# Optimization experiments

Measured on AMD Instinct MI355X. Metric: run time of the kernel, lower is better.

## Reference

```python
import jax, jax.numpy as jnp
import numpy as np

N, E, F, H, C, G = 50000, 800000, 128, 1, 64, 256
NEG_SLOPE = 0.2


def _seg_softmax(e, seg, n):
    # numerically-stable softmax over edges grouped by target node
    m = jax.ops.segment_max(e, seg, num_segments=n)
    ex = jnp.exp(e - m[seg])
    s = jax.ops.segment_sum(ex, seg, num_segments=n)
    return ex / (s[seg] + 1e-16)


def _gatv2(x, src, dst, wl, bl, wr, br, att, bo, n):
    # GATv2Conv (PyG semantics): lin_l on source x_j, lin_r on target x_i
    xl = (x @ wl.T + bl).reshape(n, H, C)
    xr = (x @ wr.T + br).reshape(n, H, C)
    s = xl[src] + xr[dst]                      # [E, H, C]
    e = jnp.sum(jax.nn.leaky_relu(s, NEG_SLOPE) * att, axis=-1)  # [E, H]
    alpha = _seg_softmax(e, dst, n)
    out = jax.ops.segment_sum(alpha[..., None] * xl[src], dst, num_segments=n)
    return out.reshape(n, H * C) + bo


def setup_inputs() -> dict:
    key = jax.random.key(0)
    ks = jax.random.split(key, 24)
    d = {}
    d['x'] = jax.random.normal(ks[0], (N, F), dtype=jnp.float32)
    d['edge_index'] = jax.random.randint(ks[1], (2, E), 0, N)
    d['batch_idx'] = jnp.sort(jax.random.randint(ks[2], (N,), 0, G))
    sc = 0.1
    # conv1: in=F, out=C
    d['wl1'] = jax.random.normal(ks[3], (H * C, F)) * sc
    d['bl1'] = jnp.zeros((H * C,), jnp.float32)
    d['wr1'] = jax.random.normal(ks[4], (H * C, F)) * sc
    d['br1'] = jnp.zeros((H * C,), jnp.float32)
    d['att1'] = jax.random.normal(ks[5], (H, C)) * sc
    d['bo1'] = jnp.zeros((H * C,), jnp.float32)
    # conv2, conv3: in=H*C, out=C
    d['wl2'] = jax.random.normal(ks[6], (H * C, H * C)) * sc
    d['bl2'] = jnp.zeros((H * C,), jnp.float32)
    d['wr2'] = jax.random.normal(ks[7], (H * C, H * C)) * sc
    d['br2'] = jnp.zeros((H * C,), jnp.float32)
    d['att2'] = jax.random.normal(ks[8], (H, C)) * sc
    d['bo2'] = jnp.zeros((H * C,), jnp.float32)
    d['wl3'] = jax.random.normal(ks[9], (H * C, H * C)) * sc
    d['bl3'] = jnp.zeros((H * C,), jnp.float32)
    d['wr3'] = jax.random.normal(ks[10], (H * C, H * C)) * sc
    d['br3'] = jnp.zeros((H * C,), jnp.float32)
    d['att3'] = jax.random.normal(ks[11], (H, C)) * sc
    d['bo3'] = jnp.zeros((H * C,), jnp.float32)
    # heads
    d['lin1_w'] = jax.random.normal(ks[12], (C, 3 * H * C)) * sc
    d['lin1_b'] = jnp.zeros((C,), jnp.float32)
    d['pred_w'] = jax.random.normal(ks[13], (C, C)) * sc
    d['pred_b'] = jnp.zeros((C,), jnp.float32)
    d['cls_w'] = jax.random.normal(ks[14], (2, C)) * sc
    d['cls_b'] = jnp.zeros((2,), jnp.float32)
    return d


def reference(x, edge_index, batch_idx, wl1, bl1, wr1, br1, att1, bo1,
              wl2, bl2, wr2, br2, att2, bo2, wl3, bl3, wr3, br3, att3, bo3,
              lin1_w, lin1_b, pred_w, pred_b, cls_w, cls_b):
    # add self-loops (GATv2Conv default add_self_loops=True)
    loop = jnp.arange(N, dtype=edge_index.dtype)
    src = jnp.concatenate([edge_index[0], loop])
    dst = jnp.concatenate([edge_index[1], loop])
    x1 = jax.nn.relu(_gatv2(x, src, dst, wl1, bl1, wr1, br1, att1, bo1, N))
    x2 = jax.nn.relu(_gatv2(x1, src, dst, wl2, bl2, wr2, br2, att2, bo2, N))
    x3 = jax.nn.relu(_gatv2(x2, src, dst, wl3, bl3, wr3, br3, att3, bo3, N))
    h = jax.nn.relu(jnp.concatenate([x1, x2, x3], axis=1) @ lin1_w.T + lin1_b)
    g = jax.ops.segment_sum(h, batch_idx, num_segments=G)  # global_add_pool
    emb = jax.nn.relu(g @ pred_w.T + pred_b)                # pred_layer
    out = emb @ cls_w.T + cls_b                             # cls_layer
    return out
```

## Files before the change

### kernel.cpp

```cpp
#include <hip/hip_runtime.h>
#include <hip/hip_bf16.h>

#define N_NODES 50000
#define N_EDGES 800000
#define FDIM 128
#define CDIM 64
#define NGRAPH 256
#define LRELU_SLOPE 0.2f
#define NBUCK ((N_NODES + 255) / 256)
#define BCAP 5120
#define ABLK 400
#define EPB ((N_EDGES + ABLK - 1) / ABLK)
#define NDBIN 64

typedef unsigned short ushort_t;
typedef unsigned int uint_t;
typedef __attribute__((ext_vector_type(8))) short short8v;
typedef __attribute__((ext_vector_type(4))) float float4v;

__device__ __forceinline__ ushort_t f2bf(float f) {
    uint_t u = __float_as_uint(f);
    u += 0x7FFFu + ((u >> 16) & 1u);
    return (ushort_t)(u >> 16);
}
__device__ __forceinline__ float bf2f(ushort_t u) {
    return __uint_as_float(((uint_t)u) << 16);
}

__device__ __forceinline__ float fast_exp2(float x) {
    return __builtin_amdgcn_exp2f(x);
}

__device__ __forceinline__ int wave_incl_scan(int v, int lane) {
#pragma unroll
    for (int off = 1; off < 64; off <<= 1) {
        int t = __shfl_up(v, off);
        if (lane >= off) v += t;
    }
    return v;
}

__device__ __forceinline__ float wave_sum(float v) {
#pragma unroll
    for (int off = 32; off >= 1; off >>= 1) v += __shfl_xor(v, off);
    return v;
}

__global__ void k_bucket(const int* __restrict__ src, const int* __restrict__ dst,
                         int* __restrict__ bcnt, int2* __restrict__ stage) {
    __shared__ int lhist[NBUCK];
    __shared__ int lbase[NBUCK];
    __shared__ int lcur[NBUCK];
    int tid = threadIdx.x;
    int e0 = blockIdx.x * EPB;
    int e1 = min(e0 + EPB, N_EDGES);
    for (int t = tid; t < NBUCK; t += 256) { lhist[t] = 0; lcur[t] = 0; }
    __syncthreads();
    for (int e = e0 + tid; e < e1; e += 256)
        atomicAdd(&lhist[dst[e] >> 8], 1);
    __syncthreads();
    for (int t = tid; t < NBUCK; t += 256)
        lbase[t] = atomicAdd(&bcnt[t], lhist[t]);
    __syncthreads();
    for (int e = e0 + tid; e < e1; e += 256) {
        int s = src[e], d = dst[e];
        int b = d >> 8;
        int loff = atomicAdd(&lcur[b], 1);
        int pos = lbase[b] + loff;
        if (pos < BCAP) stage[(size_t)b * BCAP + pos] = make_int2(s, d);
    }
}

__global__ void k_bscan(const int* __restrict__ bcnt, int* __restrict__ bbase) {
    __shared__ int wsum[4];
    int tid = threadIdx.x;
    int lane = tid & 63, w = tid >> 6;
    int v = (tid < NBUCK) ? bcnt[tid] : 0;
    int incl = wave_incl_scan(v, lane);
    if (lane == 63) wsum[w] = incl;
    __syncthreads();
    if (tid == 0) {
        int s = 0;
#pragma unroll
        for (int k = 0; k < 4; k++) { int t = wsum[k]; wsum[k] = s; s += t; }
    }
    __syncthreads();
    if (tid < NBUCK) bbase[tid] = incl - v + wsum[w];
}

__global__ void k_csr(const int* __restrict__ bcnt, const int* __restrict__ bbase,
                      const int2* __restrict__ stage, int* __restrict__ rowptr,
                      int* __restrict__ cnt, int* __restrict__ dhist,
                      int* __restrict__ csr_src) {
    __shared__ int lcnt[256];
    __shared__ int lcur[256];
    __shared__ int ldh[NDBIN];
    __shared__ int wsum[4];
    int b = blockIdx.x;
    int tid = threadIdx.x;
    int lane = tid & 63, w = tid >> 6;
    lcnt[tid] = 0;
    if (tid < NDBIN) ldh[tid] = 0;
    __syncthreads();
    int n = min(bcnt[b], BCAP);
    const int2* sp = stage + (size_t)b * BCAP;
    for (int i = tid; i < n; i += 256)
        atomicAdd(&lcnt[sp[i].y & 255], 1);
    __syncthreads();
    int v = lcnt[tid];
    int incl = wave_incl_scan(v, lane);
    if (lane == 63) wsum[w] = incl;
    __syncthreads();
    if (tid == 0) {
        int s = 0;
#pragma unroll
        for (int k = 0; k < 4; k++) { int t = wsum[k]; wsum[k] = s; s += t; }
    }
    __syncthreads();
    int excl = incl - v + wsum[w];
    int bb = bbase[b];
    int node = (b << 8) + tid;
    if (node < N_NODES) {
        rowptr[node] = bb + excl;
        cnt[node] = v;
        atomicAdd(&ldh[min(v, NDBIN - 1)], 1);
    }
    lcur[tid] = excl;
    __syncthreads();
    if (tid < NDBIN && ldh[tid]) atomicAdd(&dhist[tid], ldh[tid]);
    if (b == 0 && tid == 0) rowptr[N_NODES] = N_EDGES;
    for (int i = tid; i < n; i += 256) {
        int2 sd = sp[i];
        int pos = atomicAdd(&lcur[sd.y & 255], 1);
        csr_src[bb + pos] = sd.x;
    }
}

__global__ void k_scan2d(const int* __restrict__ dhist, int* __restrict__ dcur) {
    int lane = threadIdx.x;
    int v = dhist[lane];
    int incl = wave_incl_scan(v, lane);
    dcur[lane] = incl - v;
}

__global__ void k_dscatter(const int* __restrict__ cnt, int* __restrict__ dcur,
                           int* __restrict__ order) {
    __shared__ int lh[NDBIN], lb[NDBIN], lc[NDBIN];
    int b = blockIdx.x, tid = threadIdx.x;
    if (tid < NDBIN) { lh[tid] = 0; lc[tid] = 0; }
    __syncthreads();
    int node = b * 256 + tid;
    bool ok = node < N_NODES;
    int dg = ok ? min(cnt[node], NDBIN - 1) : 0;
    if (ok) atomicAdd(&lh[dg], 1);
    __syncthreads();
    if (tid < NDBIN) lb[tid] = lh[tid] ? atomicAdd(&dcur[tid], lh[tid]) : 0;
    __syncthreads();
    if (ok) {
        int off2 = atomicAdd(&lc[dg], 1);
        order[lb[dg] + off2] = node;
    }
}

struct WSrc {
    const float* s[7];
    int off[8];
};
__global__ void k_cvt_w(WSrc ws, ushort_t* __restrict__ hi, ushort_t* __restrict__ lo) {
    int gid = blockIdx.x * 256 + threadIdx.x;
    int stride = gridDim.x * 256;
#pragma unroll
    for (int mi = 0; mi < 7; mi++) {
        int n = ws.off[mi + 1] - ws.off[mi];
        const float* s = ws.s[mi];
        ushort_t* h = hi + ws.off[mi];
        ushort_t* l = lo + ws.off[mi];
        for (int i = gid; i < n; i += stride) {
            float f = s[i];
            ushort_t hb = f2bf(f);
            h[i] = hb;
            l[i] = f2bf(f - bf2f(hb));
        }
    }
}

template <int K, bool A_FP32>
__global__ void k_gemm_dual_mfma(const void* __restrict__ xa,
                                 const ushort_t* __restrict__ wlh, const ushort_t* __restrict__ wll,
                                 const ushort_t* __restrict__ wrh, const ushort_t* __restrict__ wrl,
                                 const float* __restrict__ bl, const float* __restrict__ br,
                                 ushort_t* __restrict__ xl, ushort_t* __restrict__ xr) {
    int tid = threadIdx.x;
    int wv = tid >> 6, lane = tid & 63;
    int m0 = blockIdx.x * 64 + wv * 16;
    if (m0 >= N_NODES) return;
    int arow = min(m0 + (lane & 15), N_NODES - 1);
    int koff = (lane >> 4) * 8;
    int wrow = lane & 15;

    float4v acc[8];
#pragma unroll
    for (int f = 0; f < 8; f++) acc[f] = (float4v)(0.f);

#pragma unroll
    for (int k0 = 0; k0 < K; k0 += 32) {
        short8v afrag;
        if (A_FP32) {
            const float* ap = (const float*)xa + (size_t)arow * K + k0 + koff;
            float4 a0 = *reinterpret_cast<const float4*>(ap);
            float4 a1 = *reinterpret_cast<const float4*>(ap + 4);
            afrag[0] = (short)f2bf(a0.x); afrag[1] = (short)f2bf(a0.y);
            afrag[2] = (short)f2bf(a0.z); afrag[3] = (short)f2bf(a0.w);
            afrag[4] = (short)f2bf(a1.x); afrag[5] = (short)f2bf(a1.y);
            afrag[6] = (short)f2bf(a1.z); afrag[7] = (short)f2bf(a1.w);
        } else {
            afrag = *reinterpret_cast<const short8v*>((const ushort_t*)xa + (size_t)arow * K + k0 + koff);
        }
#pragma unroll
        for (int f = 0; f < 8; f++) {
            const ushort_t* bh = (f < 4) ? wlh : wrh;
            const ushort_t* blo = (f < 4) ? wll : wrl;
            int row = ((f * 16 + wrow) & 63);
            size_t boff = (size_t)row * K + k0 + koff;
            short8v bfh = *reinterpret_cast<const short8v*>(bh + boff);
            short8v bfl = *reinterpret_cast<const short8v*>(blo + boff);
            acc[f] = __builtin_amdgcn_mfma_f32_16x16x32_bf16(afrag, bfh, acc[f], 0, 0, 0);
            acc[f] = __builtin_amdgcn_mfma_f32_16x16x32_bf16(afrag, bfl, acc[f], 0, 0, 0);
        }
    }

    int r0 = m0 + (lane >> 4) * 4;
#pragma unroll
    for (int f = 0; f < 8; f++) {
        int col = f * 16 + (lane & 15);
        float bias = (col < 64) ? bl[col] : br[col - 64];
        ushort_t* dstp = (col < 64) ? xl : xr;
        int c = col & 63;
#pragma unroll
        for (int j = 0; j < 4; j++) {
            int row = r0 + j;
            if (row < N_NODES) dstp[(size_t)row * 64 + c] = f2bf(acc[f][j] + bias);
        }
    }
}

__global__ void k_gemm_h_pool(const ushort_t* __restrict__ x1, const ushort_t* __restrict__ x2,
                              const ushort_t* __restrict__ x3,
                              const ushort_t* __restrict__ whi, const ushort_t* __restrict__ wlo,
                              const float* __restrict__ b, const int* __restrict__ batch,
                              float* __restrict__ g) {
    __shared__ float ht[64][65];
    int tid = threadIdx.x;
    int wv = tid >> 6, lane = tid & 63;
    int m0 = blockIdx.x * 64 + wv * 16;
    bool wactive = m0 < N_NODES;

    if (wactive) {
        int arow = min(m0 + (lane & 15), N_NODES - 1);
        int koff = (lane >> 4) * 8;
        int wrow = lane & 15;
        float4v acc[4];
#pragma unroll
        for (int f = 0; f < 4; f++) acc[f] = (float4v)(0.f);
#pragma unroll
        for (int ks = 0; ks < 6; ks++) {
            int k0 = ks * 32;
            const ushort_t* srcp = (ks < 2) ? x1 : (ks < 4 ? x2 : x3);
            int kc = k0 & 63;
            short8v afrag = *reinterpret_cast<const short8v*>(srcp + (size_t)arow * 64 + kc + koff);
#pragma unroll
            for (int f = 0; f < 4; f++) {
                size_t boff = (size_t)(f * 16 + wrow) * 192 + k0 + koff;
                short8v bfh = *reinterpret_cast<const short8v*>(whi + boff);
                short8v bfl = *reinterpret_cast<const short8v*>(wlo + boff);
                acc[f] = __builtin_amdgcn_mfma_f32_16x16x32_bf16(afrag, bfh, acc[f], 0, 0, 0);
                acc[f] = __builtin_amdgcn_mfma_f32_16x16x32_bf16(afrag, bfl, acc[f], 0, 0, 0);
            }
        }
        int r0 = wv * 16 + (lane >> 4) * 4;
#pragma unroll
        for (int f = 0; f < 4; f++) {
            int col = f * 16 + (lane & 15);
            float bias = b[col];
#pragma unroll
            for (int j = 0; j < 4; j++) {
                float o = acc[f][j] + bias;
                ht[r0 + j][col] = o > 0.f ? o : 0.f;
            }
        }
    }
    __syncthreads();

    int c = tid & 63, rr = tid >> 6;
    int blkbase = blockIdx.x * 64;
    float acc = 0.f;
    int cur = -1;
    for (int r = rr; r < 64; r += 4) {
        int node = blkbase + r;
        if (node >= N_NODES) break;
        int bb = batch[node];
        if (bb != cur) {
            if (cur >= 0) atomicAdd(&g[cur * 64 + c], acc);
            cur = bb;
            acc = 0.f;
        }
        acc += ht[r][c];
    }
    if (cur >= 0) atomicAdd(&g[cur * 64 + c], acc);
}

__global__ void k_gat(const ushort_t* __restrict__ xl, const ushort_t* __restrict__ xr,
                      const int* __restrict__ rowptr, const int* __restrict__ csr_src,
                      const int* __restrict__ order,
                      const float* __restrict__ att, const float* __restrict__ bo,
                      ushort_t* __restrict__ xout) {
    int tid = threadIdx.x;
    int wv = tid >> 6, lane = tid & 63;
    int gl = lane & 15;
    int slot = blockIdx.x * 16 + wv * 4 + (lane >> 4);
    if (slot >= N_NODES) return;
    int node = order[slot];
    const float LOG2E = 1.44269504f;
    int c0 = gl * 4;
    float4 a4 = *reinterpret_cast<const float4*>(att + c0);
    float at0 = a4.x * LOG2E, at1 = a4.y * LOG2E, at2 = a4.z * LOG2E, at3 = a4.w * LOG2E;
    size_t nb = (size_t)node * 64 + c0;
    ushort4 qr = *reinterpret_cast<const ushort4*>(xr + nb);
    ushort4 ql = *reinterpret_cast<const ushort4*>(xl + nb);
    float xr0 = bf2f(qr.x), xr1 = bf2f(qr.y), xr2 = bf2f(qr.z), xr3 = bf2f(qr.w);
    float l0 = bf2f(ql.x), l1 = bf2f(ql.y), l2 = bf2f(ql.z), l3 = bf2f(ql.w);

    auto grd = [](float p) {
        p += __shfl_xor(p, 1);
        p += __shfl_xor(p, 2);
        p += __shfl_xor(p, 4);
        p += __shfl_xor(p, 8);
        return p;
    };
    auto score4 = [&](float v0, float v1, float v2, float v3) {
        float s0 = v0 + xr0, s1 = v1 + xr1, s2 = v2 + xr2, s3 = v3 + xr3;
        float t0 = fmaxf(s0, LRELU_SLOPE * s0);
        float t1 = fmaxf(s1, LRELU_SLOPE * s1);
        float t2 = fmaxf(s2, LRELU_SLOPE * s2);
        float t3 = fmaxf(s3, LRELU_SLOPE * s3);
        return ((t0 * at0 + t1 * at1) + (t2 * at2 + t3 * at3));
    };

    int beg = rowptr[node], end = rowptr[node + 1];
    int deg = end - beg;
    int lim = end - 1;

    float m = grd(score4(l0, l1, l2, l3));
    float ssum = 1.f;
    float a0 = l0, a1 = l1, a2 = l2, a3 = l3;

    for (int j = 0; j < deg; j += 8) {
        int base = beg + j;
        int i0 = base;
        int i1 = min(base + 1, lim), i2 = min(base + 2, lim), i3 = min(base + 3, lim);
        int i4 = min(base + 4, lim), i5 = min(base + 5, lim);
        int i6 = min(base + 6, lim), i7 = min(base + 7, lim);
        int s0 = csr_src[i0], s1 = csr_src[i1], s2 = csr_src[i2], s3 = csr_src[i3];
        int s4 = csr_src[i4], s5 = csr_src[i5], s6 = csr_src[i6], s7 = csr_src[i7];
        ushort4 q0 = *reinterpret_cast<const ushort4*>(xl + (size_t)s0 * 64 + c0);
        ushort4 q1 = *reinterpret_cast<const ushort4*>(xl + (size_t)s1 * 64 + c0);
        ushort4 q2 = *reinterpret_cast<const ushort4*>(xl + (size_t)s2 * 64 + c0);
        ushort4 q3 = *reinterpret_cast<const ushort4*>(xl + (size_t)s3 * 64 + c0);
        ushort4 q4 = *reinterpret_cast<const ushort4*>(xl + (size_t)s4 * 64 + c0);
        ushort4 q5 = *reinterpret_cast<const ushort4*>(xl + (size_t)s5 * 64 + c0);
        ushort4 q6 = *reinterpret_cast<const ushort4*>(xl + (size_t)s6 * 64 + c0);
        ushort4 q7 = *reinterpret_cast<const ushort4*>(xl + (size_t)s7 * 64 + c0);
        float v00 = bf2f(q0.x), v01 = bf2f(q0.y), v02 = bf2f(q0.z), v03 = bf2f(q0.w);
        float v10 = bf2f(q1.x), v11 = bf2f(q1.y), v12 = bf2f(q1.z), v13 = bf2f(q1.w);
        float v20 = bf2f(q2.x), v21 = bf2f(q2.y), v22 = bf2f(q2.z), v23 = bf2f(q2.w);
        float v30 = bf2f(q3.x), v31 = bf2f(q3.y), v32 = bf2f(q3.z), v33 = bf2f(q3.w);
        float v40 = bf2f(q4.x), v41 = bf2f(q4.y), v42 = bf2f(q4.z), v43 = bf2f(q4.w);
        float v50 = bf2f(q5.x), v51 = bf2f(q5.y), v52 = bf2f(q5.z), v53 = bf2f(q5.w);
        float v60 = bf2f(q6.x), v61 = bf2f(q6.y), v62 = bf2f(q6.z), v63 = bf2f(q6.w);
        float v70 = bf2f(q7.x), v71 = bf2f(q7.y), v72 = bf2f(q7.z), v73 = bf2f(q7.w);
        float e0 = grd(score4(v00, v01, v02, v03));
        float e1 = grd(score4(v10, v11, v12, v13));
        float e2 = grd(score4(v20, v21, v22, v23));
        float e3 = grd(score4(v30, v31, v32, v33));
        float e4 = grd(score4(v40, v41, v42, v43));
        float e5 = grd(score4(v50, v51, v52, v53));
        float e6 = grd(score4(v60, v61, v62, v63));
        float e7 = grd(score4(v70, v71, v72, v73));
        int rem = deg - j;
        if (rem < 8) {
            e1 = (rem > 1) ? e1 : -1e30f;
            e2 = (rem > 2) ? e2 : -1e30f;
            e3 = (rem > 3) ? e3 : -1e30f;
            e4 = (rem > 4) ? e4 : -1e30f;
            e5 = (rem > 5) ? e5 : -1e30f;
            e6 = (rem > 6) ? e6 : -1e30f;
            e7 = (rem > 7) ? e7 : -1e30f;
        }
        float mx = fmaxf(fmaxf(fmaxf(e0, e1), fmaxf(e2, e3)),
                         fmaxf(fmaxf(e4, e5), fmaxf(e6, e7)));
        float mn = fmaxf(m, mx);
        float sc = fast_exp2(m - mn);
        float w0 = fast_exp2(e0 - mn), w1 = fast_exp2(e1 - mn);
        float w2 = fast_exp2(e2 - mn), w3 = fast_exp2(e3 - mn);
        float w4 = fast_exp2(e4 - mn), w5 = fast_exp2(e5 - mn);
        float w6 = fast_exp2(e6 - mn), w7 = fast_exp2(e7 - mn);
        ssum = ssum * sc + (((w0 + w1) + (w2 + w3)) + ((w4 + w5) + (w6 + w7)));
        a0 = a0 * sc + (((w0 * v00 + w1 * v10) + (w2 * v20 + w3 * v30)) +
                        ((w4 * v40 + w5 * v50) + (w6 * v60 + w7 * v70)));
        a1 = a1 * sc + (((w0 * v01 + w1 * v11) + (w2 * v21 + w3 * v31)) +
                        ((w4 * v41 + w5 * v51) + (w6 * v61 + w7 * v71)));
        a2 = a2 * sc + (((w0 * v02 + w1 * v12) + (w2 * v22 + w3 * v32)) +
                        ((w4 * v42 + w5 * v52) + (w6 * v62 + w7 * v72)));
        a3 = a3 * sc + (((w0 * v03 + w1 * v13) + (w2 * v23 + w3 * v33)) +
                        ((w4 * v43 + w5 * v53) + (w6 * v63 + w7 * v73)));
        m = mn;
    }

    float rs = 1.f / (ssum + 1e-16f);
    float4 b4 = *reinterpret_cast<const float4*>(bo + c0);
    float o0 = fmaxf(a0 * rs + b4.x, 0.f);
    float o1 = fmaxf(a1 * rs + b4.y, 0.f);
    float o2 = fmaxf(a2 * rs + b4.z, 0.f);
    float o3 = fmaxf(a3 * rs + b4.w, 0.f);
    ushort4 oq;
    oq.x = f2bf(o0); oq.y = f2bf(o1); oq.z = f2bf(o2); oq.w = f2bf(o3);
    *reinterpret_cast<ushort4*>(xout + nb) = oq;
}

__global__ void k_head(const float* __restrict__ g, const float* __restrict__ pw,
                       const float* __restrict__ pb, const float* __restrict__ cw,
                       const float* __restrict__ cb, float* __restrict__ out) {
    int gb = blockIdx.x;
    int c = threadIdx.x;
    const float* gr = g + gb * 64;
    float a = pb[c];
    const float* pwr = pw + c * 64;
#pragma unroll
    for (int k = 0; k < 64; k++) a += gr[k] * pwr[k];
    a = a > 0.f ? a : 0.f;
    float o0 = wave_sum(a * cw[c]);
    float o1 = wave_sum(a * cw[64 + c]);
    if (c == 0) {
        out[gb * 2 + 0] = o0 + cb[0];
        out[gb * 2 + 1] = o1 + cb[1];
    }
}

extern "C" void kernel_launch(void* const* d_in, const int* in_sizes, int n_in,
                              void* d_out, int out_size, void* d_ws, size_t ws_size,
                              hipStream_t stream) {
    const float* x    = (const float*)d_in[0];
    const int*   ei   = (const int*)d_in[1];
    const int*   bidx = (const int*)d_in[2];
    const float* wl1 = (const float*)d_in[3],  *bl1 = (const float*)d_in[4];
    const float* wr1 = (const float*)d_in[5],  *br1 = (const float*)d_in[6];
    const float* att1 = (const float*)d_in[7], *bo1 = (const float*)d_in[8];
    const float* wl2 = (const float*)d_in[9],  *bl2 = (const float*)d_in[10];
    const float* wr2 = (const float*)d_in[11], *br2 = (const float*)d_in[12];
    const float* att2 = (const float*)d_in[13], *bo2 = (const float*)d_in[14];
    const float* wl3 = (const float*)d_in[15], *bl3 = (const float*)d_in[16];
    const float* wr3 = (const float*)d_in[17], *br3 = (const float*)d_in[18];
    const float* att3 = (const float*)d_in[19], *bo3 = (const float*)d_in[20];
    const float* lw = (const float*)d_in[21], *lb = (const float*)d_in[22];
    const float* pw = (const float*)d_in[23], *pb = (const float*)d_in[24];
    const float* cw = (const float*)d_in[25], *cb = (const float*)d_in[26];
    float* out = (float*)d_out;

    char* wsb = (char*)d_ws;
    size_t off = 0;
    auto alloc = [&](size_t bytes) {
        void* p = wsb + off;
        off = (off + bytes + 255) & ~(size_t)255;
        return p;
    };
    int* cnt      = (int*)alloc((size_t)N_NODES * 4);
    int* rowptr   = (int*)alloc((size_t)(N_NODES + 1) * 4);
    int* bcnt     = (int*)alloc((size_t)(NBUCK + NDBIN) * 4);
    int* dhist    = bcnt + NBUCK;
    int* bbase    = (int*)alloc((size_t)NBUCK * 4);
    int* dcur     = (int*)alloc((size_t)NDBIN * 4);
    int* order    = (int*)alloc((size_t)N_NODES * 4);
    int2* stage   = (int2*)alloc((size_t)NBUCK * BCAP * 8);
    int* csr_src  = (int*)alloc((size_t)N_EDGES * 4);
    const int woff[8] = {0, 8192, 16384, 20480, 24576, 28672, 32768, 45056};
    ushort_t* whi = (ushort_t*)alloc((size_t)45056 * 2);
    ushort_t* wlo = (ushort_t*)alloc((size_t)45056 * 2);
    ushort_t* xl   = (ushort_t*)alloc((size_t)N_NODES * 64 * 2);
    ushort_t* xrr  = (ushort_t*)alloc((size_t)N_NODES * 64 * 2);
    ushort_t* x1b  = (ushort_t*)alloc((size_t)N_NODES * 64 * 2);
    ushort_t* x2b  = (ushort_t*)alloc((size_t)N_NODES * 64 * 2);
    ushort_t* x3b  = (ushort_t*)alloc((size_t)N_NODES * 64 * 2);
    float* g      = (float*)alloc((size_t)NGRAPH * 64 * 4);
    (void)ws_size; (void)in_sizes; (void)n_in; (void)out_size;

    const int* srcp = ei;
    const int* dstp = ei + N_EDGES;

    hipMemsetAsync(bcnt, 0, (size_t)(NBUCK + NDBIN) * 4, stream);
    hipMemsetAsync(g, 0, (size_t)NGRAPH * 64 * 4, stream);

    k_bucket<<<ABLK, 256, 0, stream>>>(srcp, dstp, bcnt, stage);
    k_bscan<<<1, 256, 0, stream>>>(bcnt, bbase);
    k_csr<<<NBUCK, 256, 0, stream>>>(bcnt, bbase, stage, rowptr, cnt, dhist, csr_src);
    k_scan2d<<<1, 64, 0, stream>>>(dhist, dcur);
    k_dscatter<<<NBUCK, 256, 0, stream>>>(cnt, dcur, order);

    WSrc ws;
    ws.s[0] = wl1; ws.s[1] = wr1; ws.s[2] = wl2; ws.s[3] = wr2;
    ws.s[4] = wl3; ws.s[5] = wr3; ws.s[6] = lw;
    for (int i = 0; i < 8; i++) ws.off[i] = woff[i];
    k_cvt_w<<<64, 256, 0, stream>>>(ws, whi, wlo);

    int gemmBlocks = (N_NODES + 63) / 64;
    int gatBlocks = (N_NODES + 15) / 16;

    k_gemm_dual_mfma<128, true><<<gemmBlocks, 256, 0, stream>>>(
        x, whi + woff[0], wlo + woff[0], whi + woff[1], wlo + woff[1], bl1, br1, xl, xrr);
    k_gat<<<gatBlocks, 256, 0, stream>>>(xl, xrr, rowptr, csr_src, order, att1, bo1, x1b);
    k_gemm_dual_mfma<64, false><<<gemmBlocks, 256, 0, stream>>>(
        x1b, whi + woff[2], wlo + woff[2], whi + woff[3], wlo + woff[3], bl2, br2, xl, xrr);
    k_gat<<<gatBlocks, 256, 0, stream>>>(xl, xrr, rowptr, csr_src, order, att2, bo2, x2b);
    k_gemm_dual_mfma<64, false><<<gemmBlocks, 256, 0, stream>>>(
        x2b, whi + woff[4], wlo + woff[4], whi + woff[5], wlo + woff[5], bl3, br3, xl, xrr);
    k_gat<<<gatBlocks, 256, 0, stream>>>(xl, xrr, rowptr, csr_src, order, att3, bo3, x3b);

    k_gemm_h_pool<<<gemmBlocks, 256, 0, stream>>>(x1b, x2b, x3b, whi + woff[6], wlo + woff[6],
                                                  lb, bidx, g);
    k_head<<<NGRAPH, 64, 0, stream>>>(g, pw, pb, cw, cb, out);
}
```

Measured before the change: 258.2 us.

## Split dual GEMM into left/right halves and pre-convert input to bf16

Each dual GEMM launch now uses twice as many blocks, with each half computing either the lin_l or the lin_r projection, so every wave holds 4 accumulators instead of 8. A-fragments are preloaded for all K steps. The fp32 input x is converted to bf16 once by a new kernel, so the first GEMM reads bf16. In exchange, the A matrix is read twice per layer, and the conversion adds an extra kernel launch plus a bf16 copy of x written to memory.

```diff
diff --git a/kernel.cpp b/kernel.cpp
--- a/kernel.cpp
+++ b/kernel.cpp
@@ -12,6 +12,7 @@
 #define ABLK 400
 #define EPB ((N_EDGES + ABLK - 1) / ABLK)
 #define NDBIN 64
+#define GEMMB ((N_NODES + 63) / 64)
 
 typedef unsigned short ushort_t;
 typedef unsigned int uint_t;
@@ -44,6 +45,21 @@
 #pragma unroll
     for (int off = 32; off >= 1; off >>= 1) v += __shfl_xor(v, off);
     return v;
+}
+
+__global__ void k_cvt_x(const float* __restrict__ x, ushort_t* __restrict__ xb) {
+    int i = blockIdx.x * 256 + threadIdx.x;
+    const int TOT = N_NODES * FDIM / 8;
+    if (i >= TOT) return;
+    const float* p = x + (size_t)i * 8;
+    float4 a = *reinterpret_cast<const float4*>(p);
+    float4 b = *reinterpret_cast<const float4*>(p + 4);
+    short8v o;
+    o[0] = (short)f2bf(a.x); o[1] = (short)f2bf(a.y);
+    o[2] = (short)f2bf(a.z); o[3] = (short)f2bf(a.w);
+    o[4] = (short)f2bf(b.x); o[5] = (short)f2bf(b.y);
+    o[6] = (short)f2bf(b.z); o[7] = (short)f2bf(b.w);
+    *reinterpret_cast<short8v*>(xb + (size_t)i * 8) = o;
 }
 
 __global__ void k_bucket(const int* __restrict__ src, const int* __restrict__ dst,
@@ -184,62 +200,56 @@
     }
 }
 
-template <int K, bool A_FP32>
-__global__ void k_gemm_dual_mfma(const void* __restrict__ xa,
+template <int K>
+__global__ void k_gemm_dual_mfma(const ushort_t* __restrict__ xa,
                                  const ushort_t* __restrict__ wlh, const ushort_t* __restrict__ wll,
                                  const ushort_t* __restrict__ wrh, const ushort_t* __restrict__ wrl,
                                  const float* __restrict__ bl, const float* __restrict__ br,
                                  ushort_t* __restrict__ xl, ushort_t* __restrict__ xr) {
     int tid = threadIdx.x;
     int wv = tid >> 6, lane = tid & 63;
-    int m0 = blockIdx.x * 64 + wv * 16;
+    bool rhalf = blockIdx.x >= GEMMB;
+    int blk = rhalf ? blockIdx.x - GEMMB : blockIdx.x;
+    int m0 = blk * 64 + wv * 16;
     if (m0 >= N_NODES) return;
     int arow = min(m0 + (lane & 15), N_NODES - 1);
     int koff = (lane >> 4) * 8;
     int wrow = lane & 15;
-
-    float4v acc[8];
-#pragma unroll
-    for (int f = 0; f < 8; f++) acc[f] = (float4v)(0.f);
-
-#pragma unroll
-    for (int k0 = 0; k0 < K; k0 += 32) {
-        short8v afrag;
-        if (A_FP32) {
-            const float* ap = (const float*)xa + (size_t)arow * K + k0 + koff;
-            float4 a0 = *reinterpret_cast<const float4*>(ap);
-            float4 a1 = *reinterpret_cast<const float4*>(ap + 4);
-            afrag[0] = (short)f2bf(a0.x); afrag[1] = (short)f2bf(a0.y);
-            afrag[2] = (short)f2bf(a0.z); afrag[3] = (short)f2bf(a0.w);
-            afrag[4] = (short)f2bf(a1.x); afrag[5] = (short)f2bf(a1.y);
-            afrag[6] = (short)f2bf(a1.z); afrag[7] = (short)f2bf(a1.w);
-        } else {
-            afrag = *reinterpret_cast<const short8v*>((const ushort_t*)xa + (size_t)arow * K + k0 + koff);
-        }
-#pragma unroll
-        for (int f = 0; f < 8; f++) {
-            const ushort_t* bh = (f < 4) ? wlh : wrh;
-            const ushort_t* blo = (f < 4) ? wll : wrl;
-            int row = ((f * 16 + wrow) & 63);
-            size_t boff = (size_t)row * K + k0 + koff;
+    const ushort_t* bh  = rhalf ? wrh : wlh;
+    const ushort_t* blo = rhalf ? wrl : wll;
+    const float* bias   = rhalf ? br : bl;
+    ushort_t* outp      = rhalf ? xr : xl;
+
+    short8v afrag[K / 32];
+#pragma unroll
+    for (int kk = 0; kk < K / 32; kk++)
+        afrag[kk] = *reinterpret_cast<const short8v*>(xa + (size_t)arow * K + kk * 32 + koff);
+
+    float4v acc[4];
+#pragma unroll
+    for (int f = 0; f < 4; f++) acc[f] = (float4v)(0.f);
+
+#pragma unroll
+    for (int kk = 0; kk < K / 32; kk++) {
+#pragma unroll
+        for (int f = 0; f < 4; f++) {
+            size_t boff = (size_t)(f * 16 + wrow) * K + kk * 32 + koff;
             short8v bfh = *reinterpret_cast<const short8v*>(bh + boff);
             short8v bfl = *reinterpret_cast<const short8v*>(blo + boff);
-            acc[f] = __builtin_amdgcn_mfma_f32_16x16x32_bf16(afrag, bfh, acc[f], 0, 0, 0);
-            acc[f] = __builtin_amdgcn_mfma_f32_16x16x32_bf16(afrag, bfl, acc[f], 0, 0, 0);
+            acc[f] = __builtin_amdgcn_mfma_f32_16x16x32_bf16(afrag[kk], bfh, acc[f], 0, 0, 0);
+            acc[f] = __builtin_amdgcn_mfma_f32_16x16x32_bf16(afrag[kk], bfl, acc[f], 0, 0, 0);
         }
     }
 
     int r0 = m0 + (lane >> 4) * 4;
 #pragma unroll
-    for (int f = 0; f < 8; f++) {
+    for (int f = 0; f < 4; f++) {
         int col = f * 16 + (lane & 15);
-        float bias = (col < 64) ? bl[col] : br[col - 64];
-        ushort_t* dstp = (col < 64) ? xl : xr;
-        int c = col & 63;
+        float bv = bias[col];
 #pragma unroll
         for (int j = 0; j < 4; j++) {
             int row = r0 + j;
-            if (row < N_NODES) dstp[(size_t)row * 64 + c] = f2bf(acc[f][j] + bias);
+            if (row < N_NODES) outp[(size_t)row * 64 + col] = f2bf(acc[f][j] + bv);
         }
     }
 }
@@ -485,6 +495,7 @@
     const int woff[8] = {0, 8192, 16384, 20480, 24576, 28672, 32768, 45056};
     ushort_t* whi = (ushort_t*)alloc((size_t)45056 * 2);
     ushort_t* wlo = (ushort_t*)alloc((size_t)45056 * 2);
+    ushort_t* xbf  = (ushort_t*)alloc((size_t)N_NODES * FDIM * 2);
     ushort_t* xl   = (ushort_t*)alloc((size_t)N_NODES * 64 * 2);
     ushort_t* xrr  = (ushort_t*)alloc((size_t)N_NODES * 64 * 2);
     ushort_t* x1b  = (ushort_t*)alloc((size_t)N_NODES * 64 * 2);
@@ -510,21 +521,21 @@
     ws.s[4] = wl3; ws.s[5] = wr3; ws.s[6] = lw;
     for (int i = 0; i < 8; i++) ws.off[i] = woff[i];
     k_cvt_w<<<64, 256, 0, stream>>>(ws, whi, wlo);
-
-    int gemmBlocks = (N_NODES + 63) / 64;
+    k_cvt_x<<<(N_NODES * FDIM / 8 + 255) / 256, 256, 0, stream>>>(x, xbf);
+
     int gatBlocks = (N_NODES + 15) / 16;
 
-    k_gemm_dual_mfma<128, true><<<gemmBlocks, 256, 0, stream>>>(
-        x, whi + woff[0], wlo + woff[0], whi + woff[1], wlo + woff[1], bl1, br1, xl, xrr);
+    k_gemm_dual_mfma<128><<<2 * GEMMB, 256, 0, stream>>>(
+        xbf, whi + woff[0], wlo + woff[0], whi + woff[1], wlo + woff[1], bl1, br1, xl, xrr);
     k_gat<<<gatBlocks, 256, 0, stream>>>(xl, xrr, rowptr, csr_src, order, att1, bo1, x1b);
-    k_gemm_dual_mfma<64, false><<<gemmBlocks, 256, 0, stream>>>(
+    k_gemm_dual_mfma<64><<<2 * GEMMB, 256, 0, stream>>>(
         x1b, whi + woff[2], wlo + woff[2], whi + woff[3], wlo + woff[3], bl2, br2, xl, xrr);
     k_gat<<<gatBlocks, 256, 0, stream>>>(xl, xrr, rowptr, csr_src, order, att2, bo2, x2b);
-    k_gemm_dual_mfma<64, false><<<gemmBlocks, 256, 0, stream>>>(
+    k_gemm_dual_mfma<64><<<2 * GEMMB, 256, 0, stream>>>(
         x2b, whi + woff[4], wlo + woff[4], whi + woff[5], wlo + woff[5], bl3, br3, xl, xrr);
     k_gat<<<gatBlocks, 256, 0, stream>>>(xl, xrr, rowptr, csr_src, order, att3, bo3, x3b);
 
-    k_gemm_h_pool<<<gemmBlocks, 256, 0, stream>>>(x1b, x2b, x3b, whi + woff[6], wlo + woff[6],
-                                                  lb, bidx, g);
+    k_gemm_h_pool<<<GEMMB, 256, 0, stream>>>(x1b, x2b, x3b, whi + woff[6], wlo + woff[6],
+                                             lb, bidx, g);
     k_head<<<NGRAPH, 64, 0, stream>>>(g, pw, pb, cw, cb, out);
 }
```

After: 254.0 us. Within noise of the previous version (-1.6%).
